# Kernel tuning notes

Measured on AMD Instinct MI355X. Metric: run time of the kernel, lower is better.

Reference implementation:

```python
import jax, jax.numpy as jnp
import numpy as np

NEG = -1e9

def setup_inputs() -> dict:
    key = jax.random.key(0)
    ks = jax.random.split(key, 10)
    B, T, S, D, H = 128, 64, 64, 64, 64
    A = D + H + D  # attention mlp input dim
    inp = {
        'segmented_emb': jax.random.normal(ks[0], (B, T, S, D), jnp.float32),
        'segmented_mask': jax.random.randint(ks[1], (B, T, S), 0, 2, jnp.int32),
        'target_emb': jax.random.normal(ks[2], (B, D), jnp.float32),
        'pos_w1': jax.random.normal(ks[3], (1, H), jnp.float32) * 0.3,
        'pos_b1': jnp.zeros((H,), jnp.float32),
        'pos_w2': jax.random.normal(ks[4], (H, H), jnp.float32) * (1.0 / np.sqrt(H)),
        'pos_b2': jnp.zeros((H,), jnp.float32),
        'att_w1': jax.random.normal(ks[5], (A, H), jnp.float32) * (1.0 / np.sqrt(A)),
        'att_b1': jnp.zeros((H,), jnp.float32),
        'att_w2': jax.random.normal(ks[6], (H, 1), jnp.float32) * (1.0 / np.sqrt(H)),
        'att_b2': jnp.zeros((1,), jnp.float32),
        'proj_w': jax.random.normal(ks[7], (D, D), jnp.float32) * (1.0 / np.sqrt(D)),
        'proj_b': jnp.zeros((D,), jnp.float32),
        'ln_gamma': jnp.ones((D,), jnp.float32),
        'ln_beta': jnp.zeros((D,), jnp.float32),
    }
    return inp


def reference(segmented_emb, segmented_mask, target_emb,
              pos_w1, pos_b1, pos_w2, pos_b2,
              att_w1, att_b1, att_w2, att_b2,
              proj_w, proj_b, ln_gamma, ln_beta):
    B, T, S, D = segmented_emb.shape
    # normalized positions (S, 1)
    positions = (jnp.arange(S, dtype=jnp.float32) / max(S - 1, 1))[:, None]
    # position MLP: (S, H) -- same for every (b, t)
    pos_enc = jax.nn.relu(positions @ pos_w1 + pos_b1) @ pos_w2 + pos_b2  # (S, H)
    H = pos_enc.shape[-1]
    # attention MLP layer 1 on concat([emb, pos, target]) without materializing concat:
    # split att_w1 rows into the three blocks and sum partial projections.
    w_emb, w_pos, w_tgt = att_w1[:D], att_w1[D:D + H], att_w1[D + H:]
    h = (jnp.einsum('btsd,dh->btsh', segmented_emb, w_emb)
         + (pos_enc @ w_pos)[None, None]              # (1,1,S,H)
         + (target_emb @ w_tgt)[:, None, None]        # (B,1,1,H)
         + att_b1)
    h = jax.nn.relu(h)
    scores = (h @ att_w2)[..., 0] + att_b2[0]          # (B,T,S)
    scores = jnp.where(segmented_mask == 0, NEG, scores)
    attn = jax.nn.softmax(scores, axis=-1)             # (B,T,S)
    seg = jnp.einsum('bts,btsd->btd', attn, segmented_emb)
    seg = seg @ proj_w + proj_b                        # (B,T,D)
    mu = jnp.mean(seg, axis=-1, keepdims=True)
    var = jnp.var(seg, axis=-1, keepdims=True)
    seg = (seg - mu) / jnp.sqrt(var + 1e-5) * ln_gamma + ln_beta
    return seg
```

## Files before the change

### kernel.cpp

```cpp
#include <hip/hip_runtime.h>
#include <math.h>

#define NEG_INF -1000000000.0f

__global__ __launch_bounds__(64) void doe_pre_kernel(
    const float* __restrict__ pos_w1, const float* __restrict__ pos_b1,
    const float* __restrict__ pos_w2, const float* __restrict__ pos_b2,
    const float* __restrict__ att_w1, const float* __restrict__ att_b1,
    const float* __restrict__ target_emb,
    float* __restrict__ posc, float* __restrict__ tgtc)
{
    const int tid = threadIdx.x;
    if (blockIdx.x < 64) {
        const int s = blockIdx.x;
        __shared__ float p1[64];
        __shared__ float pe[64];
        float pos = (float)s * (1.0f / 63.0f);
        p1[tid] = fmaxf(fmaf(pos, pos_w1[tid], pos_b1[tid]), 0.0f);
        __syncthreads();
        float acc = pos_b2[tid];
        #pragma unroll
        for (int h = 0; h < 64; ++h) acc = fmaf(p1[h], pos_w2[h * 64 + tid], acc);
        pe[tid] = acc;
        __syncthreads();
        float pc = att_b1[tid];
        #pragma unroll
        for (int h = 0; h < 64; ++h) pc = fmaf(pe[h], att_w1[(64 + h) * 64 + tid], pc);
        posc[s * 64 + tid] = pc;
    } else {
        const int b = blockIdx.x - 64;
        const float* trow = target_emb + b * 64;
        float acc = 0.0f;
        #pragma unroll
        for (int d = 0; d < 64; ++d) acc = fmaf(trow[d], att_w1[(128 + d) * 64 + tid], acc);
        tgtc[b * 64 + tid] = acc;
    }
}

__global__ __launch_bounds__(256, 2) void doe_main_kernel(
    const float* __restrict__ seg_emb, const int* __restrict__ smask,
    const float* __restrict__ att_w1, const float* __restrict__ att_w2,
    const float* __restrict__ att_b2, const float* __restrict__ proj_w,
    const float* __restrict__ proj_b, const float* __restrict__ ln_g,
    const float* __restrict__ ln_b, const float* __restrict__ posc,
    const float* __restrict__ tgtc, float* __restrict__ out)
{
    __shared__ float tile[4][4096];
    __shared__ float attn_s[4][64];
    __shared__ float segv_s[4][64];

    const int w    = threadIdx.x >> 6;
    const int lane = threadIdx.x & 63;
    const int g    = (blockIdx.x << 2) | w;
    const int b    = g >> 6;

    float* tl = tile[w];

    {
        const float4* src4 = (const float4*)(seg_emb + (size_t)g * 4096);
        float4* tl4 = (float4*)tl;
        #pragma unroll
        for (int i = 0; i < 16; ++i) {
            int q = (i << 6) | lane;
            float4 v = src4[q];
            int s = q >> 4, u = q & 15;
            tl4[(s << 4) | (u ^ (s & 7))] = v;
        }
    }

    const int s = lane;
    const int mval = smask[(g << 6) | s];

    __syncthreads();

    float acc[64];
    {
        const float* pr = posc + s * 64;
        const float* tr = tgtc + b * 64;
        #pragma unroll
        for (int j = 0; j < 64; ++j) acc[j] = pr[j] + tr[j];
    }
    const float4* tl4 = (const float4*)tl;
    const int sw = s & 7;
    float4 a = tl4[(s << 4) | (0 ^ sw)];
    #pragma unroll 1
    for (int dc = 0; dc < 15; ++dc) {
        float4 nxt = tl4[(s << 4) | ((dc + 1) ^ sw)];
        const float* w0 = att_w1 + (dc << 8);
        #pragma unroll
        for (int j = 0; j < 64; ++j) {
            float t0 = fmaf(a.w, w0[192 + j], acc[j]);
            t0 = fmaf(a.z, w0[128 + j], t0);
            t0 = fmaf(a.y, w0[64 + j], t0);
            acc[j] = fmaf(a.x, w0[j], t0);
        }
        a = nxt;
    }
    {
        const float* w0 = att_w1 + (15 << 8);
        #pragma unroll
        for (int j = 0; j < 64; ++j) {
            float t0 = fmaf(a.w, w0[192 + j], acc[j]);
            t0 = fmaf(a.z, w0[128 + j], t0);
            t0 = fmaf(a.y, w0[64 + j], t0);
            acc[j] = fmaf(a.x, w0[j], t0);
        }
    }

    float sc = att_b2[0];
    #pragma unroll
    for (int j = 0; j < 64; ++j) sc = fmaf(fmaxf(acc[j], 0.0f), att_w2[j], sc);
    if (mval == 0) sc = NEG_INF;

    float mx = sc;
    #pragma unroll
    for (int off = 32; off; off >>= 1) mx = fmaxf(mx, __shfl_xor(mx, off));
    float e = __expf(sc - mx);
    float sum = e;
    #pragma unroll
    for (int off = 32; off; off >>= 1) sum += __shfl_xor(sum, off);
    attn_s[w][lane] = e / sum;
    __syncthreads();

    const int d = lane;
    float segv = 0.0f;
    #pragma unroll
    for (int s2 = 0; s2 < 64; ++s2) {
        float av = attn_s[w][s2];
        float tv = tl[(s2 << 6) | ((((d >> 2) ^ (s2 & 7)) << 2) | (d & 3))];
        segv = fmaf(av, tv, segv);
    }
    segv_s[w][d] = segv;
    __syncthreads();

    float o = proj_b[d];
    #pragma unroll
    for (int d2 = 0; d2 < 64; ++d2)
        o = fmaf(segv_s[w][d2], proj_w[(d2 << 6) | d], o);

    float ssum = o;
    #pragma unroll
    for (int off = 32; off; off >>= 1) ssum += __shfl_xor(ssum, off);
    float mu = ssum * (1.0f / 64.0f);
    float df = o - mu;
    float vsum = df * df;
    #pragma unroll
    for (int off = 32; off; off >>= 1) vsum += __shfl_xor(vsum, off);
    float var = vsum * (1.0f / 64.0f);
    float inv = 1.0f / sqrtf(var + 1e-5f);
    out[(g << 6) | d] = fmaf(df * inv, ln_g[d], ln_b[d]);
}

extern "C" void kernel_launch(void* const* d_in, const int* in_sizes, int n_in,
                              void* d_out, int out_size, void* d_ws, size_t ws_size,
                              hipStream_t stream)
{
    const float* seg_emb    = (const float*)d_in[0];
    const int*   smask      = (const int*)  d_in[1];
    const float* target_emb = (const float*)d_in[2];
    const float* pos_w1     = (const float*)d_in[3];
    const float* pos_b1     = (const float*)d_in[4];
    const float* pos_w2     = (const float*)d_in[5];
    const float* pos_b2     = (const float*)d_in[6];
    const float* att_w1     = (const float*)d_in[7];
    const float* att_b1     = (const float*)d_in[8];
    const float* att_w2     = (const float*)d_in[9];
    const float* att_b2     = (const float*)d_in[10];
    const float* proj_w     = (const float*)d_in[11];
    const float* proj_b     = (const float*)d_in[12];
    const float* ln_g       = (const float*)d_in[13];
    const float* ln_b       = (const float*)d_in[14];
    float* out = (float*)d_out;

    float* posc = (float*)d_ws;
    float* tgtc = posc + 4096;

    doe_pre_kernel<<<192, 64, 0, stream>>>(pos_w1, pos_b1, pos_w2, pos_b2,
                                           att_w1, att_b1, target_emb, posc, tgtc);
    doe_main_kernel<<<2048, 256, 0, stream>>>(seg_emb, smask, att_w1, att_w2,
                                              att_b2, proj_w, proj_b, ln_g, ln_b,
                                              posc, tgtc, out);
}
```

Measured before the change: 284.3 us.

## Drop LDS tile staging; load rows directly to registers and use shuffles

Removes the 64KB shared-memory tile and the block-wide barriers. Each lane now loads its own 256-byte row of segmented_emb straight from global memory in float4 chunks, prefetched a few chunks ahead. The weighted sum re-reads columns from global (likely hitting cache) and exchanges attention weights and seg vectors through wave shuffles instead of LDS. Launch bounds rise to 4 blocks per CU to raise occupancy. The trade-offs are strided, uncoalesced row loads per lane, a second read of each tile from global, and tighter register limits that could cause spills with the 64-float accumulator.

```diff
diff --git a/kernel.cpp b/kernel.cpp
--- a/kernel.cpp
+++ b/kernel.cpp
@@ -37,7 +37,19 @@
     }
 }
 
-__global__ __launch_bounds__(256, 2) void doe_main_kernel(
+__device__ __forceinline__ void fma4rows(float acc[64], const float4 a,
+                                         const float* __restrict__ w0)
+{
+    #pragma unroll
+    for (int j = 0; j < 64; ++j) {
+        float t0 = fmaf(a.w, w0[192 + j], acc[j]);
+        t0 = fmaf(a.z, w0[128 + j], t0);
+        t0 = fmaf(a.y, w0[64 + j], t0);
+        acc[j] = fmaf(a.x, w0[j], t0);
+    }
+}
+
+__global__ __launch_bounds__(256, 4) void doe_main_kernel(
     const float* __restrict__ seg_emb, const int* __restrict__ smask,
     const float* __restrict__ att_w1, const float* __restrict__ att_w2,
     const float* __restrict__ att_b2, const float* __restrict__ proj_w,
@@ -45,66 +57,48 @@
     const float* __restrict__ ln_b, const float* __restrict__ posc,
     const float* __restrict__ tgtc, float* __restrict__ out)
 {
-    __shared__ float tile[4][4096];
-    __shared__ float attn_s[4][64];
-    __shared__ float segv_s[4][64];
-
     const int w    = threadIdx.x >> 6;
     const int lane = threadIdx.x & 63;
     const int g    = (blockIdx.x << 2) | w;
     const int b    = g >> 6;
+    const int s    = lane;
 
-    float* tl = tile[w];
+    const float4* rp4 = (const float4*)(seg_emb + (size_t)g * 4096 + s * 64);
+    float4 c0 = rp4[0], c1 = rp4[1], c2 = rp4[2], c3 = rp4[3];
 
+    const int mval = smask[(g << 6) | s];
+
+    float acc[64];
     {
-        const float4* src4 = (const float4*)(seg_emb + (size_t)g * 4096);
-        float4* tl4 = (float4*)tl;
+        const float4* pp4 = (const float4*)(posc + s * 64);
+        const float*  tr  = tgtc + b * 64;
         #pragma unroll
-        for (int i = 0; i < 16; ++i) {
-            int q = (i << 6) | lane;
-            float4 v = src4[q];
-            int s = q >> 4, u = q & 15;
-            tl4[(s << 4) | (u ^ (s & 7))] = v;
+        for (int jq = 0; jq < 16; ++jq) {
+            float4 pv = pp4[jq];
+            acc[4 * jq + 0] = pv.x + tr[4 * jq + 0];
+            acc[4 * jq + 1] = pv.y + tr[4 * jq + 1];
+            acc[4 * jq + 2] = pv.z + tr[4 * jq + 2];
+            acc[4 * jq + 3] = pv.w + tr[4 * jq + 3];
         }
     }
 
-    const int s = lane;
-    const int mval = smask[(g << 6) | s];
-
-    __syncthreads();
-
-    float acc[64];
-    {
-        const float* pr = posc + s * 64;
-        const float* tr = tgtc + b * 64;
-        #pragma unroll
-        for (int j = 0; j < 64; ++j) acc[j] = pr[j] + tr[j];
-    }
-    const float4* tl4 = (const float4*)tl;
-    const int sw = s & 7;
-    float4 a = tl4[(s << 4) | (0 ^ sw)];
     #pragma unroll 1
-    for (int dc = 0; dc < 15; ++dc) {
-        float4 nxt = tl4[(s << 4) | ((dc + 1) ^ sw)];
-        const float* w0 = att_w1 + (dc << 8);
-        #pragma unroll
-        for (int j = 0; j < 64; ++j) {
-            float t0 = fmaf(a.w, w0[192 + j], acc[j]);
-            t0 = fmaf(a.z, w0[128 + j], t0);
-            t0 = fmaf(a.y, w0[64 + j], t0);
-            acc[j] = fmaf(a.x, w0[j], t0);
-        }
-        a = nxt;
+    for (int dq = 0; dq < 3; ++dq) {
+        float4 n0 = rp4[4 * dq + 4], n1 = rp4[4 * dq + 5];
+        float4 n2 = rp4[4 * dq + 6], n3 = rp4[4 * dq + 7];
+        const float* wq = att_w1 + dq * 1024;
+        fma4rows(acc, c0, wq);
+        fma4rows(acc, c1, wq + 256);
+        fma4rows(acc, c2, wq + 512);
+        fma4rows(acc, c3, wq + 768);
+        c0 = n0; c1 = n1; c2 = n2; c3 = n3;
     }
     {
-        const float* w0 = att_w1 + (15 << 8);
-        #pragma unroll
-        for (int j = 0; j < 64; ++j) {
-            float t0 = fmaf(a.w, w0[192 + j], acc[j]);
-            t0 = fmaf(a.z, w0[128 + j], t0);
-            t0 = fmaf(a.y, w0[64 + j], t0);
-            acc[j] = fmaf(a.x, w0[j], t0);
-        }
+        const float* wq = att_w1 + 3 * 1024;
+        fma4rows(acc, c0, wq);
+        fma4rows(acc, c1, wq + 256);
+        fma4rows(acc, c2, wq + 512);
+        fma4rows(acc, c3, wq + 768);
     }
 
     float sc = att_b2[0];
@@ -119,24 +113,22 @@
     float sum = e;
     #pragma unroll
     for (int off = 32; off; off >>= 1) sum += __shfl_xor(sum, off);
-    attn_s[w][lane] = e / sum;
-    __syncthreads();
+    const float p = e / sum;
 
-    const int d = lane;
+    const float* colb = seg_emb + (size_t)g * 4096 + lane;
     float segv = 0.0f;
     #pragma unroll
     for (int s2 = 0; s2 < 64; ++s2) {
-        float av = attn_s[w][s2];
-        float tv = tl[(s2 << 6) | ((((d >> 2) ^ (s2 & 7)) << 2) | (d & 3))];
-        segv = fmaf(av, tv, segv);
+        float av = __shfl(p, s2);
+        segv = fmaf(av, colb[s2 * 64], segv);
     }
-    segv_s[w][d] = segv;
-    __syncthreads();
 
-    float o = proj_b[d];
+    float o = proj_b[lane];
     #pragma unroll
-    for (int d2 = 0; d2 < 64; ++d2)
-        o = fmaf(segv_s[w][d2], proj_w[(d2 << 6) | d], o);
+    for (int d2 = 0; d2 < 64; ++d2) {
+        float sv = __shfl(segv, d2);
+        o = fmaf(sv, proj_w[d2 * 64 + lane], o);
+    }
 
     float ssum = o;
     #pragma unroll
@@ -148,7 +140,7 @@
     for (int off = 32; off; off >>= 1) vsum += __shfl_xor(vsum, off);
     float var = vsum * (1.0f / 64.0f);
     float inv = 1.0f / sqrtf(var + 1e-5f);
-    out[(g << 6) | d] = fmaf(df * inv, ln_g[d], ln_b[d]);
+    out[(g << 6) | lane] = fmaf(df * inv, ln_g[lane], ln_b[lane]);
 }
 
 extern "C" void kernel_launch(void* const* d_in, const int* in_sizes, int n_in,
```

After: 263.2 us. 7.4% less time.
